# Performance work log

Measured on AMD Instinct MI355X. Metric: run time of the kernel, lower is better.

## Reference

```python
import jax, jax.numpy as jnp
import numpy as np

DIM, HEADS, WH, WW, NPROMPT, NW, BATCH = 384, 12, 7, 7, 5, 64, 32
N = WH * WW + NPROMPT  # 54


def _make_rel_index():
    ch, cw = np.meshgrid(np.arange(WH), np.arange(WW), indexing='ij')
    coords = np.stack([ch, cw]).reshape(2, -1)  # [2, 49]
    rel = coords[:, :, None] - coords[:, None, :]  # [2,49,49]
    rel = rel.transpose(1, 2, 0)
    rel[:, :, 0] += WH - 1
    rel[:, :, 1] += WW - 1
    rel[:, :, 0] *= 2 * WW - 1
    return rel.sum(-1).astype(np.int32)  # [49,49]


def setup_inputs() -> dict:
    key = jax.random.key(0)
    ks = jax.random.split(key, 7)
    B_ = BATCH * NW
    x = jax.random.normal(ks[0], (B_, N, DIM), jnp.float32)
    # 0/-inf style shifted-window mask; random floats exercise the same math
    mask = jnp.where(jax.random.uniform(ks[1], (NW, WH * WW, WH * WW)) > 0.8,
                     jnp.float32(-100.0), jnp.float32(0.0))
    qkv_w = 0.02 * jax.random.normal(ks[2], (3 * DIM, DIM), jnp.float32)
    qkv_b = 0.02 * jax.random.normal(ks[3], (3 * DIM,), jnp.float32)
    proj_w = 0.02 * jax.random.normal(ks[4], (DIM, DIM), jnp.float32)
    proj_b = 0.02 * jax.random.normal(ks[5], (DIM,), jnp.float32)
    rpb_table = 0.02 * jax.random.normal(ks[6], ((2 * WH - 1) * (2 * WW - 1), HEADS), jnp.float32)
    rel_index = jnp.asarray(_make_rel_index())
    return {"x": x, "mask": mask, "qkv_w": qkv_w, "qkv_b": qkv_b,
            "proj_w": proj_w, "proj_b": proj_b, "rpb_table": rpb_table,
            "rel_index": rel_index}


def reference(x, mask, qkv_w, qkv_b, proj_w, proj_b, rpb_table, rel_index):
    B_, n, C = x.shape
    hd = C // HEADS
    scale = hd ** -0.5
    qkv = (x @ qkv_w.T + qkv_b).reshape(B_, n, 3, HEADS, hd)
    qkv = jnp.moveaxis(qkv, 2, 0)  # [3, B_, n, H, hd]
    q, k, v = qkv[0], qkv[1], qkv[2]  # [B_, n, H, hd]
    attn = jnp.einsum('bnhd,bmhd->bhnm', q * scale, k)  # [B_, H, n, n]
    nw2 = WH * WW
    bias = rpb_table[rel_index.reshape(-1)].reshape(nw2, nw2, HEADS)
    bias = jnp.transpose(bias, (2, 0, 1))  # [H, 49, 49]
    bias = jnp.pad(bias, ((0, 0), (NPROMPT, 0), (NPROMPT, 0)))  # [H, n, n]
    attn = attn + bias[None]
    nW = mask.shape[0]
    mask_p = jnp.pad(mask, ((0, 0), (NPROMPT, 0), (NPROMPT, 0)))  # [nW, n, n]
    attn = attn.reshape(B_ // nW, nW, HEADS, n, n) + mask_p[None, :, None]
    attn = jax.nn.softmax(attn.reshape(B_, HEADS, n, n), axis=-1)
    out = jnp.einsum('bhnm,bmhd->bnhd', attn, v).reshape(B_, n, C)
    return out @ proj_w.T + proj_b
```

## Files before the change

kernel.cpp:

```cpp
#include <hip/hip_runtime.h>

#define DIM 384
#define NH 12
#define NT 54
#define NWIN 64
#define MTOT 110592
#define HS ((size_t)MTOT * 32)

typedef __attribute__((ext_vector_type(8))) short short8;
typedef __attribute__((ext_vector_type(4))) float f32x4;

__device__ __forceinline__ unsigned short f2bf(float f) {
  unsigned int u = __float_as_uint(f);
  u += 0x7fffu + ((u >> 16) & 1u);
  return (unsigned short)(u >> 16);
}
__device__ __forceinline__ float bf2f(unsigned short s) {
  return __uint_as_float((unsigned int)s << 16);
}

__global__ __launch_bounds__(256) void convert_x(
    const float* __restrict__ x, unsigned short* __restrict__ xb) {
  const size_t i8 = ((size_t)blockIdx.x * 256 + threadIdx.x) * 8;
  float4 fa = *(const float4*)&x[i8];
  float4 fb = *(const float4*)&x[i8 + 4];
  short8 s;
  s[0] = f2bf(fa.x); s[1] = f2bf(fa.y); s[2] = f2bf(fa.z); s[3] = f2bf(fa.w);
  s[4] = f2bf(fb.x); s[5] = f2bf(fb.y); s[6] = f2bf(fb.z); s[7] = f2bf(fb.w);
  *(short8*)&xb[i8] = s;
}

__global__ __launch_bounds__(256) void prep2_kernel(
    const float* __restrict__ qkv_w, const float* __restrict__ proj_w,
    const float* __restrict__ mask, const float* __restrict__ rpb,
    const int* __restrict__ rel,
    unsigned short* __restrict__ Wq, unsigned short* __restrict__ Wp,
    unsigned short* __restrict__ bmt) {
  int idx = blockIdx.x * 256 + threadIdx.x;
  if (idx < 1152 * 384) { Wq[idx] = f2bf(qkv_w[idx]); return; }
  idx -= 1152 * 384;
  if (idx < 384 * 384) { Wp[idx] = f2bf(proj_w[idx]); return; }
  idx -= 384 * 384;
  if (idx < NWIN * NH * 64 * 64) {
    int w = idx / (NH * 4096);
    int rem = idx - w * (NH * 4096);
    int h = rem >> 12, r = (rem >> 6) & 63, c = rem & 63;
    float v;
    if (r >= NT || c >= NT) v = -1e30f;
    else if (r >= 5 && c >= 5)
      v = rpb[rel[(r - 5) * 49 + (c - 5)] * NH + h] +
          mask[w * 2401 + (r - 5) * 49 + (c - 5)];
    else v = 0.0f;
    bmt[w * (NH * 4096) + (h << 12) + (c << 6) + r] = f2bf(v);
  }
}

__global__ __launch_bounds__(256) void qkv_gemm2(
    const unsigned short* __restrict__ xb, const unsigned short* __restrict__ Wq,
    const float* __restrict__ qkv_b,
    unsigned short* __restrict__ Qb, unsigned short* __restrict__ Kb,
    unsigned short* __restrict__ Vb) {
  __shared__ unsigned short As[128][72];
  __shared__ unsigned short Bs[128][72];
  const int s = blockIdx.x;
  const int xcd = s & 7, slot = s >> 3;
  const size_t m0 = (size_t)(xcd * 108 + slot / 9) * 128;
  const int n0 = (slot % 9) * 128;
  const int tid = threadIdx.x;
  const int wv = tid >> 6, ln = tid & 63, g = ln >> 4, lc = ln & 15;
  const int wr = (wv >> 1) * 64, wc = (wv & 1) * 64;
  f32x4 acc[4][4];
#pragma unroll
  for (int i = 0; i < 4; ++i)
#pragma unroll
    for (int j = 0; j < 4; ++j) acc[i][j] = (f32x4){0.f, 0.f, 0.f, 0.f};

  const int srow = tid >> 3, l8 = tid & 7;
  for (int kc = 0; kc < 6; ++kc) {
    const int k0 = kc * 64;
#pragma unroll
    for (int it = 0; it < 4; ++it) {
      const int r = srow + it * 32;
      *(short8*)&As[r][l8 * 8] =
          *(const short8*)&xb[(m0 + r) * 384 + k0 + l8 * 8];
      *(short8*)&Bs[r][l8 * 8] =
          *(const short8*)&Wq[(size_t)(n0 + r) * 384 + k0 + l8 * 8];
    }
    __syncthreads();
#pragma unroll
    for (int kk = 0; kk < 2; ++kk) {
      short8 af[4], bfr[4];
#pragma unroll
      for (int ms = 0; ms < 4; ++ms)
        af[ms] = *(const short8*)&As[wr + ms * 16 + lc][kk * 32 + g * 8];
#pragma unroll
      for (int ns = 0; ns < 4; ++ns)
        bfr[ns] = *(const short8*)&Bs[wc + ns * 16 + lc][kk * 32 + g * 8];
#pragma unroll
      for (int ms = 0; ms < 4; ++ms)
#pragma unroll
        for (int ns = 0; ns < 4; ++ns)
          acc[ms][ns] = __builtin_amdgcn_mfma_f32_16x16x32_bf16(
              af[ms], bfr[ns], acc[ms][ns], 0, 0, 0);
    }
    __syncthreads();
  }
  const int sel = n0 / 384;
  const float factor = (sel == 0) ? 0.17677669529663687f : 1.0f;
  unsigned short* outp = (sel == 0) ? Qb : (sel == 1 ? Kb : Vb);
#pragma unroll
  for (int ns = 0; ns < 4; ++ns) {
    const int n = n0 + wc + ns * 16 + lc;
    const int rel = n - sel * 384;
    const int h = rel >> 5, d = rel & 31;
    const float bias = qkv_b[n];
#pragma unroll
    for (int ms = 0; ms < 4; ++ms)
#pragma unroll
      for (int rr = 0; rr < 4; ++rr) {
        const size_t m = m0 + wr + ms * 16 + g * 4 + rr;
        outp[(size_t)h * HS + m * 32 + d] = f2bf((acc[ms][ns][rr] + bias) * factor);
      }
  }
}

__global__ __launch_bounds__(256) void attn2_kernel(
    unsigned short* __restrict__ Qb, const unsigned short* __restrict__ Kb,
    const unsigned short* __restrict__ Vb, const unsigned short* __restrict__ bmt) {
  __shared__ unsigned short Ps[NT][72];
  __shared__ unsigned short vT[32][72];
  const int s = blockIdx.x;
  const int xcd = s & 7, slot = s >> 3;
  const int b = xcd * 256 + slot / 12;
  const int h = slot - 12 * (slot / 12);
  const int tid = threadIdx.x;
  const int wv = tid >> 6, ln = tid & 63, g = ln >> 4, lc = ln & 15;
  const int m0 = wv * 16, wi = b & 63;
  const size_t base = (size_t)b * NT;
  const int arow = (m0 + lc < NT) ? (m0 + lc) : (NT - 1);
  unsigned short* Qh = Qb + (size_t)h * HS;
  const unsigned short* Kh = Kb + (size_t)h * HS;
  const unsigned short* Vh = Vb + (size_t)h * HS;

  for (int i = tid; i < 320; i += 256) {
    int d = i / 10, m = NT + (i - d * 10);
    vT[d][m] = 0;
  }

  const int vr = tid >> 2, vc = (tid & 3) * 8;
  short8 vv;
  if (tid < 216)
    vv = *(const short8*)&Vh[(base + vr) * 32 + vc];

  short8 a = *(const short8*)&Qh[(base + arow) * 32 + g * 8];
  const unsigned short* bmh = &bmt[(size_t)(wi * NH + h) << 12];
  const int row0 = m0 + g * 4;
  f32x4 sac[4];
#pragma unroll
  for (int t = 0; t < 4; ++t) {
    const int col = t * 16 + lc;
    const int kr = (col < NT) ? col : (NT - 1);
    short8 kb = *(const short8*)&Kh[(base + kr) * 32 + g * 8];
    uint2 uu = *(const uint2*)&bmh[(col << 6) + row0];
    f32x4 c0;
    c0[0] = bf2f((unsigned short)(uu.x & 0xffffu));
    c0[1] = bf2f((unsigned short)(uu.x >> 16));
    c0[2] = bf2f((unsigned short)(uu.y & 0xffffu));
    c0[3] = bf2f((unsigned short)(uu.y >> 16));
    sac[t] = __builtin_amdgcn_mfma_f32_16x16x32_bf16(a, kb, c0, 0, 0, 0);
  }
  float rmax[4] = {-3.0e38f, -3.0e38f, -3.0e38f, -3.0e38f};
#pragma unroll
  for (int t = 0; t < 4; ++t)
#pragma unroll
    for (int rr = 0; rr < 4; ++rr) rmax[rr] = fmaxf(rmax[rr], sac[t][rr]);
#pragma unroll
  for (int rr = 0; rr < 4; ++rr)
#pragma unroll
    for (int off = 1; off < 16; off <<= 1)
      rmax[rr] = fmaxf(rmax[rr], __shfl_xor(rmax[rr], off));
  float rsum[4] = {0.f, 0.f, 0.f, 0.f};
#pragma unroll
  for (int t = 0; t < 4; ++t)
#pragma unroll
    for (int rr = 0; rr < 4; ++rr) {
      float p = __expf(sac[t][rr] - rmax[rr]);
      sac[t][rr] = p;
      rsum[rr] += p;
    }
#pragma unroll
  for (int rr = 0; rr < 4; ++rr) {
#pragma unroll
    for (int off = 1; off < 16; off <<= 1)
      rsum[rr] += __shfl_xor(rsum[rr], off);
    rsum[rr] = 1.0f / rsum[rr];
  }
#pragma unroll
  for (int t = 0; t < 4; ++t)
#pragma unroll
    for (int rr = 0; rr < 4; ++rr) {
      const int row = row0 + rr;
      if (row < NT) Ps[row][t * 16 + lc] = f2bf(sac[t][rr] * rsum[rr]);
    }
  if (tid < 216) {
#pragma unroll
    for (int j = 0; j < 8; ++j) vT[vc + j][vr] = (unsigned short)vv[j];
  }
  __syncthreads();
  f32x4 oac[2];
  oac[0] = (f32x4){0.f, 0.f, 0.f, 0.f};
  oac[1] = (f32x4){0.f, 0.f, 0.f, 0.f};
#pragma unroll
  for (int k2 = 0; k2 < 2; ++k2) {
    short8 pa = *(const short8*)&Ps[arow][k2 * 32 + g * 8];
#pragma unroll
    for (int tn = 0; tn < 2; ++tn) {
      short8 vb = *(const short8*)&vT[tn * 16 + lc][k2 * 32 + g * 8];
      oac[tn] = __builtin_amdgcn_mfma_f32_16x16x32_bf16(pa, vb, oac[tn], 0, 0, 0);
    }
  }
#pragma unroll
  for (int tn = 0; tn < 2; ++tn) {
    const int d = tn * 16 + lc;
#pragma unroll
    for (int rr = 0; rr < 4; ++rr) {
      const int m = m0 + g * 4 + rr;
      if (m < NT) Qh[(base + m) * 32 + d] = f2bf(oac[tn][rr]);
    }
  }
}

__global__ __launch_bounds__(256) void proj_hmajor(
    const unsigned short* __restrict__ AO, const unsigned short* __restrict__ Wp,
    const float* __restrict__ proj_b, float* __restrict__ out) {
  __shared__ unsigned short As[128][72];
  __shared__ unsigned short Bs[128][72];
  const int s = blockIdx.x;
  const int xcd = s & 7, slot = s >> 3;
  const size_t m0 = (size_t)(xcd * 108 + slot / 3) * 128;
  const int n0 = (slot % 3) * 128;
  const int tid = threadIdx.x;
  const int wv = tid >> 6, ln = tid & 63, g = ln >> 4, lc = ln & 15;
  const int wr = (wv >> 1) * 64, wc = (wv & 1) * 64;
  f32x4 acc[4][4];
#pragma unroll
  for (int i = 0; i < 4; ++i)
#pragma unroll
    for (int j = 0; j < 4; ++j) acc[i][j] = (f32x4){0.f, 0.f, 0.f, 0.f};

  const int srow = tid >> 3, l8 = tid & 7;
  for (int kc = 0; kc < 6; ++kc) {
    const int k0 = kc * 64;
    const int kg = k0 + l8 * 8;
    const int hh = kg >> 5, dd = kg & 31;
#pragma unroll
    for (int it = 0; it < 4; ++it) {
      const int r = srow + it * 32;
      *(short8*)&As[r][l8 * 8] =
          *(const short8*)&AO[(size_t)hh * HS + (m0 + r) * 32 + dd];
      *(short8*)&Bs[r][l8 * 8] =
          *(const short8*)&Wp[(size_t)(n0 + r) * 384 + k0 + l8 * 8];
    }
    __syncthreads();
#pragma unroll
    for (int kk = 0; kk < 2; ++kk) {
      short8 af[4], bfr[4];
#pragma unroll
      for (int ms = 0; ms < 4; ++ms)
        af[ms] = *(const short8*)&As[wr + ms * 16 + lc][kk * 32 + g * 8];
#pragma unroll
      for (int ns = 0; ns < 4; ++ns)
        bfr[ns] = *(const short8*)&Bs[wc + ns * 16 + lc][kk * 32 + g * 8];
#pragma unroll
      for (int ms = 0; ms < 4; ++ms)
#pragma unroll
        for (int ns = 0; ns < 4; ++ns)
          acc[ms][ns] = __builtin_amdgcn_mfma_f32_16x16x32_bf16(
              af[ms], bfr[ns], acc[ms][ns], 0, 0, 0);
    }
    __syncthreads();
  }
#pragma unroll
  for (int ns = 0; ns < 4; ++ns) {
    const int n = n0 + wc + ns * 16 + lc;
    const float pb = proj_b[n];
#pragma unroll
    for (int ms = 0; ms < 4; ++ms)
#pragma unroll
      for (int rr = 0; rr < 4; ++rr) {
        const size_t m = m0 + wr + ms * 16 + g * 4 + rr;
        out[m * 384 + n] = acc[ms][ns][rr] + pb;
      }
  }
}

__global__ __launch_bounds__(256) void prep_kernel(
    const float* __restrict__ qkv_w, const float* __restrict__ proj_w,
    const float* __restrict__ mask, const float* __restrict__ rpb,
    const int* __restrict__ rel,
    unsigned short* __restrict__ Wq, unsigned short* __restrict__ Wp,
    float* __restrict__ bias_tab, float* __restrict__ maskp) {
  int idx = blockIdx.x * 256 + threadIdx.x;
  if (idx < 1152 * 384) { Wq[idx] = f2bf(qkv_w[idx]); return; }
  idx -= 1152 * 384;
  if (idx < 384 * 384) { Wp[idx] = f2bf(proj_w[idx]); return; }
  idx -= 384 * 384;
  if (idx < NH * 64 * 64) {
    int h = idx >> 12, r = (idx >> 6) & 63, c = idx & 63;
    float v;
    if (r >= NT || c >= NT) v = -1e30f;
    else if (r >= 5 && c >= 5) v = rpb[rel[(r - 5) * 49 + (c - 5)] * NH + h];
    else v = 0.0f;
    bias_tab[idx] = v;
    return;
  }
  idx -= NH * 64 * 64;
  if (idx < NWIN * 64 * 64) {
    int w = idx >> 12, r = (idx >> 6) & 63, c = idx & 63;
    float v = 0.0f;
    if (r >= 5 && r < NT && c >= 5 && c < NT)
      v = mask[w * 2401 + (r - 5) * 49 + (c - 5)];
    maskp[idx] = v;
  }
}

__global__ __launch_bounds__(256) void fused_attn(
    const float* __restrict__ x, const unsigned short* __restrict__ Wq,
    const float* __restrict__ qkv_b, const float* __restrict__ bias_tab,
    const float* __restrict__ maskp, unsigned short* __restrict__ AO) {
  __shared__ unsigned short xs[NT][392];
  __shared__ unsigned short qs[NT][40];
  __shared__ unsigned short ksm[NT][40];
  __shared__ unsigned short vT[32][72];
  __shared__ unsigned short Ps[NT][72];
  const int b = blockIdx.x;
  const int tid = threadIdx.x;
  const int wv = tid >> 6, ln = tid & 63;
  const int g = ln >> 4, lc = ln & 15;
  const int m0 = wv * 16;
  const int wi = b & 63;
  const float scale = 0.17677669529663687f;
  const float* xb = x + (size_t)b * (NT * DIM);
  for (int i = tid; i < NT * DIM / 4; i += 256) {
    float4 v = ((const float4*)xb)[i];
    int e = i * 4, r = e / DIM, c = e - r * DIM;
    unsigned short* p = &xs[r][c];
    p[0] = f2bf(v.x); p[1] = f2bf(v.y); p[2] = f2bf(v.z); p[3] = f2bf(v.w);
  }
  __syncthreads();
  const int arow = (m0 + lc < NT) ? (m0 + lc) : (NT - 1);
  for (int h = 0; h < NH; ++h) {
    f32x4 acc[6];
#pragma unroll
    for (int t = 0; t < 6; ++t) acc[t] = (f32x4){0.f, 0.f, 0.f, 0.f};
#pragma unroll 2
    for (int kk = 0; kk < 12; ++kk) {
      short8 a = *(const short8*)&xs[arow][kk * 32 + g * 8];
#pragma unroll
      for (int t = 0; t < 6; ++t) {
        const int sel = t >> 1;
        const int wrow = sel * 384 + h * 32 + (t & 1) * 16 + lc;
        short8 bfr = *(const short8*)&Wq[wrow * 384 + kk * 32 + g * 8];
        acc[t] = __builtin_amdgcn_mfma_f32_16x16x32_bf16(a, bfr, acc[t], 0, 0, 0);
      }
    }
#pragma unroll
    for (int t = 0; t < 6; ++t) {
      const int sel = t >> 1;
      const int d = (t & 1) * 16 + lc;
      const float bias = qkv_b[sel * 384 + h * 32 + d];
#pragma unroll
      for (int r = 0; r < 4; ++r) {
        const int m = m0 + g * 4 + r;
        float v = acc[t][r] + bias;
        if (sel == 2) vT[d][m] = f2bf(v);
        else if (m < NT) {
          if (sel == 0) qs[m][d] = f2bf(v * scale);
          else ksm[m][d] = f2bf(v);
        }
      }
    }
    __syncthreads();
    f32x4 sac[4];
    {
      short8 a = *(const short8*)&qs[arow][g * 8];
#pragma unroll
      for (int t = 0; t < 4; ++t) {
        const int kr = (t * 16 + lc < NT) ? (t * 16 + lc) : (NT - 1);
        short8 bfr = *(const short8*)&ksm[kr][g * 8];
        sac[t] = __builtin_amdgcn_mfma_f32_16x16x32_bf16(
            a, bfr, (f32x4){0.f, 0.f, 0.f, 0.f}, 0, 0, 0);
      }
    }
    const float* bt = bias_tab + h * 4096;
    const float* mp = maskp + wi * 4096;
    float sv[4][4];
    float rmax[4];
#pragma unroll
    for (int r = 0; r < 4; ++r) rmax[r] = -3.0e38f;
#pragma unroll
    for (int t = 0; t < 4; ++t) {
      const int col = t * 16 + lc;
#pragma unroll
      for (int r = 0; r < 4; ++r) {
        const int row = m0 + g * 4 + r;
        float s = sac[t][r] + bt[row * 64 + col] + mp[row * 64 + col];
        sv[t][r] = s;
        rmax[r] = fmaxf(rmax[r], s);
      }
    }
#pragma unroll
    for (int r = 0; r < 4; ++r)
#pragma unroll
      for (int off = 1; off < 16; off <<= 1)
        rmax[r] = fmaxf(rmax[r], __shfl_xor(rmax[r], off));
    float rsum[4] = {0.f, 0.f, 0.f, 0.f};
#pragma unroll
    for (int t = 0; t < 4; ++t)
#pragma unroll
      for (int r = 0; r < 4; ++r) {
        float p = __expf(sv[t][r] - rmax[r]);
        sv[t][r] = p;
        rsum[r] += p;
      }
#pragma unroll
    for (int r = 0; r < 4; ++r) {
#pragma unroll
      for (int off = 1; off < 16; off <<= 1)
        rsum[r] += __shfl_xor(rsum[r], off);
      rsum[r] = 1.0f / rsum[r];
    }
#pragma unroll
    for (int t = 0; t < 4; ++t) {
      const int col = t * 16 + lc;
#pragma unroll
      for (int r = 0; r < 4; ++r) {
        const int row = m0 + g * 4 + r;
        if (row < NT) Ps[row][col] = f2bf(sv[t][r] * rsum[r]);
      }
    }
    __syncthreads();
    f32x4 oac[2];
    oac[0] = (f32x4){0.f, 0.f, 0.f, 0.f};
    oac[1] = (f32x4){0.f, 0.f, 0.f, 0.f};
#pragma unroll
    for (int k2 = 0; k2 < 2; ++k2) {
      short8 a = *(const short8*)&Ps[arow][k2 * 32 + g * 8];
#pragma unroll
      for (int tn = 0; tn < 2; ++tn) {
        short8 bfr = *(const short8*)&vT[tn * 16 + lc][k2 * 32 + g * 8];
        oac[tn] = __builtin_amdgcn_mfma_f32_16x16x32_bf16(a, bfr, oac[tn], 0, 0, 0);
      }
    }
    unsigned short* aob = AO + (size_t)b * (NT * DIM) + h * 32;
#pragma unroll
    for (int tn = 0; tn < 2; ++tn) {
      const int d = tn * 16 + lc;
#pragma unroll
      for (int r = 0; r < 4; ++r) {
        const int m = m0 + g * 4 + r;
        if (m < NT) aob[m * DIM + d] = f2bf(oac[tn][r]);
      }
    }
    __syncthreads();
  }
}

__global__ __launch_bounds__(256) void proj_kernel(
    const unsigned short* __restrict__ AO, const unsigned short* __restrict__ Wp,
    const float* __restrict__ proj_b, float* __restrict__ out, int lda) {
  __shared__ unsigned short As[128][72];
  __shared__ unsigned short Bs[128][72];
  const int s = blockIdx.x;
  const int xcd = s & 7, slot = s >> 3;
  const size_t m0 = (size_t)(xcd * 108 + slot / 3) * 128;
  const int n0 = (slot % 3) * 128;
  const int tid = threadIdx.x;
  const int wv = tid >> 6, ln = tid & 63, g = ln >> 4, lc = ln & 15;
  const int wr = (wv >> 1) * 64, wc = (wv & 1) * 64;
  f32x4 acc[4][4];
#pragma unroll
  for (int i = 0; i < 4; ++i)
#pragma unroll
    for (int j = 0; j < 4; ++j) acc[i][j] = (f32x4){0.f, 0.f, 0.f, 0.f};

  const int srow = tid >> 3, l8 = tid & 7;
  for (int kc = 0; kc < 6; ++kc) {
    const int k0 = kc * 64;
#pragma unroll
    for (int it = 0; it < 4; ++it) {
      const int r = srow + it * 32;
      *(short8*)&As[r][l8 * 8] =
          *(const short8*)&AO[(m0 + r) * (size_t)lda + k0 + l8 * 8];
      *(short8*)&Bs[r][l8 * 8] =
          *(const short8*)&Wp[(size_t)(n0 + r) * 384 + k0 + l8 * 8];
    }
    __syncthreads();
#pragma unroll
    for (int kk = 0; kk < 2; ++kk) {
      short8 af[4], bfr[4];
#pragma unroll
      for (int ms = 0; ms < 4; ++ms)
        af[ms] = *(const short8*)&As[wr + ms * 16 + lc][kk * 32 + g * 8];
#pragma unroll
      for (int ns = 0; ns < 4; ++ns)
        bfr[ns] = *(const short8*)&Bs[wc + ns * 16 + lc][kk * 32 + g * 8];
#pragma unroll
      for (int ms = 0; ms < 4; ++ms)
#pragma unroll
        for (int ns = 0; ns < 4; ++ns)
          acc[ms][ns] = __builtin_amdgcn_mfma_f32_16x16x32_bf16(
              af[ms], bfr[ns], acc[ms][ns], 0, 0, 0);
    }
    __syncthreads();
  }
#pragma unroll
  for (int ns = 0; ns < 4; ++ns) {
    const int n = n0 + wc + ns * 16 + lc;
    const float pb = proj_b[n];
#pragma unroll
    for (int ms = 0; ms < 4; ++ms)
#pragma unroll
      for (int rr = 0; rr < 4; ++rr) {
        const size_t m = m0 + wr + ms * 16 + g * 4 + rr;
        out[m * 384 + n] = acc[ms][ns][rr] + pb;
      }
  }
}

extern "C" void kernel_launch(void* const* d_in, const int* in_sizes, int n_in,
                              void* d_out, int out_size, void* d_ws, size_t ws_size,
                              hipStream_t stream) {
  const float* x      = (const float*)d_in[0];
  const float* mask   = (const float*)d_in[1];
  const float* qkv_w  = (const float*)d_in[2];
  const float* qkv_b  = (const float*)d_in[3];
  const float* proj_w = (const float*)d_in[4];
  const float* proj_b = (const float*)d_in[5];
  const float* rpb    = (const float*)d_in[6];
  const int*   rel    = (const int*)d_in[7];
  float* out = (float*)d_out;

  const size_t QKV_ELEMS = (size_t)3 * NH * HS;
  const size_t WQ_ELEMS = 1152 * 384, WP_ELEMS = 384 * 384;
  const size_t BMT_ELEMS = (size_t)NWIN * NH * 4096;
  const size_t need = (QKV_ELEMS + WQ_ELEMS + WP_ELEMS + BMT_ELEMS) * 2;

  if (ws_size >= need) {
    unsigned short* Qb  = (unsigned short*)d_ws;
    unsigned short* Kb  = Qb + NH * HS;
    unsigned short* Vb  = Kb + NH * HS;
    unsigned short* Wq  = Vb + NH * HS;
    unsigned short* Wp  = Wq + WQ_ELEMS;
    unsigned short* bmt = Wp + WP_ELEMS;
    unsigned short* xb = (unsigned short*)d_out;

    convert_x<<<20736, 256, 0, stream>>>(x, xb);
    prep2_kernel<<<14592, 256, 0, stream>>>(qkv_w, proj_w, mask, rpb, rel,
                                            Wq, Wp, bmt);
    qkv_gemm2<<<7776, 256, 0, stream>>>(xb, Wq, qkv_b, Qb, Kb, Vb);
    attn2_kernel<<<24576, 256, 0, stream>>>(Qb, Kb, Vb, bmt);
    proj_hmajor<<<2592, 256, 0, stream>>>(Qb, Wp, proj_b, out);
  } else {
    unsigned short* Wq = (unsigned short*)d_ws;
    unsigned short* Wp = Wq + 442368;
    float* bias_tab = (float*)(Wp + 147456);
    float* maskp = bias_tab + 12 * 64 * 64;
    unsigned short* AO = (unsigned short*)(maskp + 64 * 64 * 64);
    prep_kernel<<<3520, 256, 0, stream>>>(qkv_w, proj_w, mask, rpb, rel,
                                          Wq, Wp, bias_tab, maskp);
    fused_attn<<<2048, 256, 0, stream>>>(x, Wq, qkv_b, bias_tab, maskp, AO);
    proj_kernel<<<2592, 256, 0, stream>>>(AO, Wp, proj_b, out, 384);
  }
}
```

Before: 419.8 us.

## Fuse x conversion into QKV GEMM, double-buffer GEMM tiles, remap attention blocks

Removes the separate fp32-to-bf16 pass over x. The QKV GEMM now reads fp32 x directly and converts it with v_cvt_pk_bf16_f32 while staging into LDS. Both GEMMs get double-buffered LDS with register prefetch of the next K-chunk, which drops one barrier per iteration and overlaps global loads with MFMA. Attention block indexing is remapped so each XCD handles a fixed set of windows and reuses their bias/mask tiles in cache, and packed bf16 conversion replaces the software rounding. In exchange, the GEMM reads twice as many bytes of x from HBM and doubles its LDS footprint, which may lower occupancy.

```diff
diff --git a/kernel.cpp b/kernel.cpp
--- a/kernel.cpp
+++ b/kernel.cpp
@@ -18,16 +18,10 @@
 __device__ __forceinline__ float bf2f(unsigned short s) {
   return __uint_as_float((unsigned int)s << 16);
 }
-
-__global__ __launch_bounds__(256) void convert_x(
-    const float* __restrict__ x, unsigned short* __restrict__ xb) {
-  const size_t i8 = ((size_t)blockIdx.x * 256 + threadIdx.x) * 8;
-  float4 fa = *(const float4*)&x[i8];
-  float4 fb = *(const float4*)&x[i8 + 4];
-  short8 s;
-  s[0] = f2bf(fa.x); s[1] = f2bf(fa.y); s[2] = f2bf(fa.z); s[3] = f2bf(fa.w);
-  s[4] = f2bf(fb.x); s[5] = f2bf(fb.y); s[6] = f2bf(fb.z); s[7] = f2bf(fb.w);
-  *(short8*)&xb[i8] = s;
+__device__ __forceinline__ unsigned int cvtpk(float a, float b) {
+  unsigned int r;
+  asm("v_cvt_pk_bf16_f32 %0, %1, %2" : "=v"(r) : "v"(a), "v"(b));
+  return r;
 }
 
 __global__ __launch_bounds__(256) void prep2_kernel(
@@ -55,13 +49,13 @@
   }
 }
 
-__global__ __launch_bounds__(256) void qkv_gemm2(
-    const unsigned short* __restrict__ xb, const unsigned short* __restrict__ Wq,
+__global__ __launch_bounds__(256) void qkv_gemm3(
+    const float* __restrict__ x, const unsigned short* __restrict__ Wq,
     const float* __restrict__ qkv_b,
     unsigned short* __restrict__ Qb, unsigned short* __restrict__ Kb,
     unsigned short* __restrict__ Vb) {
-  __shared__ unsigned short As[128][72];
-  __shared__ unsigned short Bs[128][72];
+  __shared__ unsigned short As[2][128][72];
+  __shared__ unsigned short Bs[2][128][72];
   const int s = blockIdx.x;
   const int xcd = s & 7, slot = s >> 3;
   const size_t m0 = (size_t)(xcd * 108 + slot / 9) * 128;
@@ -69,58 +63,92 @@
   const int tid = threadIdx.x;
   const int wv = tid >> 6, ln = tid & 63, g = ln >> 4, lc = ln & 15;
   const int wr = (wv >> 1) * 64, wc = (wv & 1) * 64;
+  const int srow = tid >> 3, l8 = tid & 7;
+
+  float4 xa[4], xc[4];
+  short8 brg[4];
   f32x4 acc[4][4];
 #pragma unroll
   for (int i = 0; i < 4; ++i)
 #pragma unroll
     for (int j = 0; j < 4; ++j) acc[i][j] = (f32x4){0.f, 0.f, 0.f, 0.f};
 
-  const int srow = tid >> 3, l8 = tid & 7;
+#define QKV_ISSUE(kc_) do {                                              \
+    const int k0_ = (kc_) * 64;                                          \
+    _Pragma("unroll")                                                    \
+    for (int it = 0; it < 4; ++it) {                                     \
+      const int r_ = srow + it * 32;                                     \
+      const float* ap_ = &x[(m0 + r_) * 384 + k0_ + l8 * 8];             \
+      xa[it] = *(const float4*)ap_;                                      \
+      xc[it] = *(const float4*)(ap_ + 4);                                \
+      brg[it] = *(const short8*)&Wq[(size_t)(n0 + r_) * 384 + k0_ + l8 * 8]; \
+    } } while (0)
+
+#define QKV_WRITE(buf_) do {                                             \
+    _Pragma("unroll")                                                    \
+    for (int it = 0; it < 4; ++it) {                                     \
+      const int r_ = srow + it * 32;                                     \
+      uint4 u_;                                                          \
+      u_.x = cvtpk(xa[it].x, xa[it].y);                                  \
+      u_.y = cvtpk(xa[it].z, xa[it].w);                                  \
+      u_.z = cvtpk(xc[it].x, xc[it].y);                                  \
+      u_.w = cvtpk(xc[it].z, xc[it].w);                                  \
+      *(uint4*)&As[buf_][r_][l8 * 8] = u_;                               \
+      *(short8*)&Bs[buf_][r_][l8 * 8] = brg[it];                         \
+    } } while (0)
+
+  QKV_ISSUE(0);
+  QKV_WRITE(0);
+#pragma unroll
   for (int kc = 0; kc < 6; ++kc) {
-    const int k0 = kc * 64;
-#pragma unroll
-    for (int it = 0; it < 4; ++it) {
-      const int r = srow + it * 32;
-      *(short8*)&As[r][l8 * 8] =
-          *(const short8*)&xb[(m0 + r) * 384 + k0 + l8 * 8];
-      *(short8*)&Bs[r][l8 * 8] =
-          *(const short8*)&Wq[(size_t)(n0 + r) * 384 + k0 + l8 * 8];
-    }
+    const int cur = kc & 1;
     __syncthreads();
+    if (kc < 5) QKV_ISSUE(kc + 1);
 #pragma unroll
     for (int kk = 0; kk < 2; ++kk) {
-      short8 af[4], bfr[4];
+      short8 af[4], bfv[4];
 #pragma unroll
       for (int ms = 0; ms < 4; ++ms)
-        af[ms] = *(const short8*)&As[wr + ms * 16 + lc][kk * 32 + g * 8];
+        af[ms] = *(const short8*)&As[cur][wr + ms * 16 + lc][kk * 32 + g * 8];
 #pragma unroll
       for (int ns = 0; ns < 4; ++ns)
-        bfr[ns] = *(const short8*)&Bs[wc + ns * 16 + lc][kk * 32 + g * 8];
+        bfv[ns] = *(const short8*)&Bs[cur][wc + ns * 16 + lc][kk * 32 + g * 8];
 #pragma unroll
       for (int ms = 0; ms < 4; ++ms)
 #pragma unroll
         for (int ns = 0; ns < 4; ++ns)
           acc[ms][ns] = __builtin_amdgcn_mfma_f32_16x16x32_bf16(
-              af[ms], bfr[ns], acc[ms][ns], 0, 0, 0);
-    }
-    __syncthreads();
-  }
+              af[ms], bfv[ns], acc[ms][ns], 0, 0, 0);
+    }
+    if (kc < 5) QKV_WRITE(cur ^ 1);
+  }
+#undef QKV_ISSUE
+#undef QKV_WRITE
+
   const int sel = n0 / 384;
   const float factor = (sel == 0) ? 0.17677669529663687f : 1.0f;
   unsigned short* outp = (sel == 0) ? Qb : (sel == 1 ? Kb : Vb);
 #pragma unroll
   for (int ns = 0; ns < 4; ++ns) {
     const int n = n0 + wc + ns * 16 + lc;
-    const int rel = n - sel * 384;
-    const int h = rel >> 5, d = rel & 31;
+    const int rl = n - sel * 384;
+    const int h = rl >> 5, d = rl & 31;
     const float bias = qkv_b[n];
 #pragma unroll
-    for (int ms = 0; ms < 4; ++ms)
-#pragma unroll
-      for (int rr = 0; rr < 4; ++rr) {
-        const size_t m = m0 + wr + ms * 16 + g * 4 + rr;
-        outp[(size_t)h * HS + m * 32 + d] = f2bf((acc[ms][ns][rr] + bias) * factor);
-      }
+    for (int ms = 0; ms < 4; ++ms) {
+      const size_t mrow = m0 + wr + ms * 16 + g * 4;
+      const float v0 = (acc[ms][ns][0] + bias) * factor;
+      const float v1 = (acc[ms][ns][1] + bias) * factor;
+      const float v2 = (acc[ms][ns][2] + bias) * factor;
+      const float v3 = (acc[ms][ns][3] + bias) * factor;
+      const unsigned int u01 = cvtpk(v0, v1);
+      const unsigned int u23 = cvtpk(v2, v3);
+      unsigned short* p = &outp[(size_t)h * HS + mrow * 32 + d];
+      p[0]  = (unsigned short)(u01 & 0xffffu);
+      p[32] = (unsigned short)(u01 >> 16);
+      p[64] = (unsigned short)(u23 & 0xffffu);
+      p[96] = (unsigned short)(u23 >> 16);
+    }
   }
 }
 
@@ -130,12 +158,15 @@
   __shared__ unsigned short Ps[NT][72];
   __shared__ unsigned short vT[32][72];
   const int s = blockIdx.x;
-  const int xcd = s & 7, slot = s >> 3;
-  const int b = xcd * 256 + slot / 12;
-  const int h = slot - 12 * (slot / 12);
+  const int xcd = s & 7, r3 = s >> 3;
+  const int h = r3 % 12;
+  const int t2 = r3 / 12;
+  const int batch = t2 & 31;
+  const int w = xcd * 8 + (t2 >> 5);
+  const int b = batch * 64 + w;
   const int tid = threadIdx.x;
   const int wv = tid >> 6, ln = tid & 63, g = ln >> 4, lc = ln & 15;
-  const int m0 = wv * 16, wi = b & 63;
+  const int m0 = wv * 16;
   const size_t base = (size_t)b * NT;
   const int arow = (m0 + lc < NT) ? (m0 + lc) : (NT - 1);
   unsigned short* Qh = Qb + (size_t)h * HS;
@@ -153,7 +184,7 @@
     vv = *(const short8*)&Vh[(base + vr) * 32 + vc];
 
   short8 a = *(const short8*)&Qh[(base + arow) * 32 + g * 8];
-  const unsigned short* bmh = &bmt[(size_t)(wi * NH + h) << 12];
+  const unsigned short* bmh = &bmt[(size_t)(w * NH + h) << 12];
   const int row0 = m0 + g * 4;
   f32x4 sac[4];
 #pragma unroll
@@ -196,12 +227,15 @@
     rsum[rr] = 1.0f / rsum[rr];
   }
 #pragma unroll
-  for (int t = 0; t < 4; ++t)
-#pragma unroll
-    for (int rr = 0; rr < 4; ++rr) {
-      const int row = row0 + rr;
-      if (row < NT) Ps[row][t * 16 + lc] = f2bf(sac[t][rr] * rsum[rr]);
-    }
+  for (int t = 0; t < 4; ++t) {
+    const int col = t * 16 + lc;
+    const unsigned int u01 = cvtpk(sac[t][0] * rsum[0], sac[t][1] * rsum[1]);
+    const unsigned int u23 = cvtpk(sac[t][2] * rsum[2], sac[t][3] * rsum[3]);
+    if (row0 < NT)     Ps[row0][col]     = (unsigned short)(u01 & 0xffffu);
+    if (row0 + 1 < NT) Ps[row0 + 1][col] = (unsigned short)(u01 >> 16);
+    if (row0 + 2 < NT) Ps[row0 + 2][col] = (unsigned short)(u23 & 0xffffu);
+    if (row0 + 3 < NT) Ps[row0 + 3][col] = (unsigned short)(u23 >> 16);
+  }
   if (tid < 216) {
 #pragma unroll
     for (int j = 0; j < 8; ++j) vT[vc + j][vr] = (unsigned short)vv[j];
@@ -222,19 +256,21 @@
 #pragma unroll
   for (int tn = 0; tn < 2; ++tn) {
     const int d = tn * 16 + lc;
-#pragma unroll
-    for (int rr = 0; rr < 4; ++rr) {
-      const int m = m0 + g * 4 + rr;
-      if (m < NT) Qh[(base + m) * 32 + d] = f2bf(oac[tn][rr]);
-    }
+    const unsigned int u01 = cvtpk(oac[tn][0], oac[tn][1]);
+    const unsigned int u23 = cvtpk(oac[tn][2], oac[tn][3]);
+    unsigned short* p = &Qh[(base + row0) * 32 + d];
+    if (row0 < NT)     p[0]  = (unsigned short)(u01 & 0xffffu);
+    if (row0 + 1 < NT) p[32] = (unsigned short)(u01 >> 16);
+    if (row0 + 2 < NT) p[64] = (unsigned short)(u23 & 0xffffu);
+    if (row0 + 3 < NT) p[96] = (unsigned short)(u23 >> 16);
   }
 }
 
 __global__ __launch_bounds__(256) void proj_hmajor(
     const unsigned short* __restrict__ AO, const unsigned short* __restrict__ Wp,
     const float* __restrict__ proj_b, float* __restrict__ out) {
-  __shared__ unsigned short As[128][72];
-  __shared__ unsigned short Bs[128][72];
+  __shared__ unsigned short As[2][128][72];
+  __shared__ unsigned short Bs[2][128][72];
   const int s = blockIdx.x;
   const int xcd = s & 7, slot = s >> 3;
   const size_t m0 = (size_t)(xcd * 108 + slot / 3) * 128;
@@ -242,44 +278,61 @@
   const int tid = threadIdx.x;
   const int wv = tid >> 6, ln = tid & 63, g = ln >> 4, lc = ln & 15;
   const int wr = (wv >> 1) * 64, wc = (wv & 1) * 64;
+  const int srow = tid >> 3, l8 = tid & 7;
+
+  short8 arg[4], brg[4];
   f32x4 acc[4][4];
 #pragma unroll
   for (int i = 0; i < 4; ++i)
 #pragma unroll
     for (int j = 0; j < 4; ++j) acc[i][j] = (f32x4){0.f, 0.f, 0.f, 0.f};
 
-  const int srow = tid >> 3, l8 = tid & 7;
+#define PRJ_ISSUE(kc_) do {                                              \
+    const int kg_ = (kc_) * 64 + l8 * 8;                                 \
+    const int hh_ = kg_ >> 5, dd_ = kg_ & 31;                            \
+    _Pragma("unroll")                                                    \
+    for (int it = 0; it < 4; ++it) {                                     \
+      const int r_ = srow + it * 32;                                     \
+      arg[it] = *(const short8*)&AO[(size_t)hh_ * HS + (m0 + r_) * 32 + dd_]; \
+      brg[it] = *(const short8*)&Wp[(size_t)(n0 + r_) * 384 + kg_];      \
+    } } while (0)
+
+#define PRJ_WRITE(buf_) do {                                             \
+    _Pragma("unroll")                                                    \
+    for (int it = 0; it < 4; ++it) {                                     \
+      const int r_ = srow + it * 32;                                     \
+      *(short8*)&As[buf_][r_][l8 * 8] = arg[it];                         \
+      *(short8*)&Bs[buf_][r_][l8 * 8] = brg[it];                         \
+    } } while (0)
+
+  PRJ_ISSUE(0);
+  PRJ_WRITE(0);
+#pragma unroll
   for (int kc = 0; kc < 6; ++kc) {
-    const int k0 = kc * 64;
-    const int kg = k0 + l8 * 8;
-    const int hh = kg >> 5, dd = kg & 31;
-#pragma unroll
-    for (int it = 0; it < 4; ++it) {
-      const int r = srow + it * 32;
-      *(short8*)&As[r][l8 * 8] =
-          *(const short8*)&AO[(size_t)hh * HS + (m0 + r) * 32 + dd];
-      *(short8*)&Bs[r][l8 * 8] =
-          *(const short8*)&Wp[(size_t)(n0 + r) * 384 + k0 + l8 * 8];
-    }
+    const int cur = kc & 1;
     __syncthreads();
+    if (kc < 5) PRJ_ISSUE(kc + 1);
 #pragma unroll
     for (int kk = 0; kk < 2; ++kk) {
-      short8 af[4], bfr[4];
+      short8 af[4], bfv[4];
 #pragma unroll
       for (int ms = 0; ms < 4; ++ms)
-        af[ms] = *(const short8*)&As[wr + ms * 16 + lc][kk * 32 + g * 8];
+        af[ms] = *(const short8*)&As[cur][wr + ms * 16 + lc][kk * 32 + g * 8];
 #pragma unroll
       for (int ns = 0; ns < 4; ++ns)
-        bfr[ns] = *(const short8*)&Bs[wc + ns * 16 + lc][kk * 32 + g * 8];
+        bfv[ns] = *(const short8*)&Bs[cur][wc + ns * 16 + lc][kk * 32 + g * 8];
 #pragma unroll
       for (int ms = 0; ms < 4; ++ms)
 #pragma unroll
         for (int ns = 0; ns < 4; ++ns)
           acc[ms][ns] = __builtin_amdgcn_mfma_f32_16x16x32_bf16(
-              af[ms], bfr[ns], acc[ms][ns], 0, 0, 0);
-    }
-    __syncthreads();
-  }
+              af[ms], bfv[ns], acc[ms][ns], 0, 0, 0);
+    }
+    if (kc < 5) PRJ_WRITE(cur ^ 1);
+  }
+#undef PRJ_ISSUE
+#undef PRJ_WRITE
+
 #pragma unroll
   for (int ns = 0; ns < 4; ++ns) {
     const int n = n0 + wc + ns * 16 + lc;
@@ -553,12 +606,10 @@
     unsigned short* Wq  = Vb + NH * HS;
     unsigned short* Wp  = Wq + WQ_ELEMS;
     unsigned short* bmt = Wp + WP_ELEMS;
-    unsigned short* xb = (unsigned short*)d_out;
-
-    convert_x<<<20736, 256, 0, stream>>>(x, xb);
+
     prep2_kernel<<<14592, 256, 0, stream>>>(qkv_w, proj_w, mask, rpb, rel,
                                             Wq, Wp, bmt);
-    qkv_gemm2<<<7776, 256, 0, stream>>>(xb, Wq, qkv_b, Qb, Kb, Vb);
+    qkv_gemm3<<<7776, 256, 0, stream>>>(x, Wq, qkv_b, Qb, Kb, Vb);
     attn2_kernel<<<24576, 256, 0, stream>>>(Qb, Kb, Vb, bmt);
     proj_hmajor<<<2592, 256, 0, stream>>>(Qb, Wp, proj_b, out);
   } else {
```

After: 459.0 us. 1.09x slower.
